# Optimization experiments

Measured on AMD Instinct MI355X. Metric: run time of the kernel, lower is better.

## Reference

```python
import jax, jax.numpy as jnp
import numpy as np

TOKENS = 1024
HIDDEN = 1024
INTER = 4096
N_EXPERTS = 8


def setup_inputs() -> dict:
    key = jax.random.key(0)
    k1, k2, k3, k4 = jax.random.split(key, 4)
    hidden_states = jax.random.normal(k1, (TOKENS, HIDDEN), dtype=jnp.float32)
    # multi-hot expert assignment mask [tokens, num_experts] with values in {0,1}
    expert_indices = jax.random.randint(k2, (TOKENS, N_EXPERTS), 0, 2, dtype=jnp.int32)
    # Phi3MLP weights per expert (Linear layers have bias=False in Phi3)
    scale_gu = 1.0 / np.sqrt(HIDDEN)
    scale_d = 1.0 / np.sqrt(INTER)
    w_gate_up = jax.random.normal(k3, (N_EXPERTS, HIDDEN, 2 * INTER), dtype=jnp.float32) * scale_gu
    w_down = jax.random.normal(k4, (N_EXPERTS, INTER, HIDDEN), dtype=jnp.float32) * scale_d
    return {
        "hidden_states": hidden_states,
        "expert_indices": expert_indices,
        "w_gate_up": w_gate_up,
        "w_down": w_down,
    }


def reference(hidden_states, expert_indices, w_gate_up, w_down):
    # Original loops per expert: gather masked tokens, run Phi3MLP, scatter-add back.
    # Mathematically equivalent dense form (jit-friendly, static shapes):
    #   out = sum_e mask[:, e] * Phi3MLP_e(x)
    # gate_up: [E, T, 2*I]
    gu = jnp.einsum('th,ehi->eti', hidden_states, w_gate_up)
    gate, up = jnp.split(gu, 2, axis=-1)  # each [E, T, I]
    act = up * jax.nn.silu(gate)          # Phi3MLP: up * silu(gate)
    y = jnp.einsum('eti,eih->eth', act, w_down)  # [E, T, H]
    mask = expert_indices.astype(hidden_states.dtype)  # [T, E]
    out = jnp.einsum('eth,te->th', y, mask)
    return out
```

## Files before the change

kernel.cpp:

```cpp
#include <hip/hip_runtime.h>
#include <hip/hip_bf16.h>
#include <stdint.h>

#define T_TOK 1024
#define HID   1024
#define INT_  4096
#define NE    8

typedef __attribute__((ext_vector_type(4))) float f32x4;
typedef __attribute__((ext_vector_type(8))) short short8;

__device__ int g_tok[NE][T_TOK];
__device__ int g_cnt[NE];

__device__ __forceinline__ uint32_t pack2bf(float a, float b) {
  unsigned short ua = __builtin_bit_cast(unsigned short, (__bf16)a);
  unsigned short ub = __builtin_bit_cast(unsigned short, (__bf16)b);
  return (uint32_t)ua | ((uint32_t)ub << 16);
}

__global__ void k0_compact(const int* __restrict__ mask)
{
  const int w    = threadIdx.x >> 6;
  const int lane = threadIdx.x & 63;
  if (w >= NE) return;
  const unsigned long long ltmask = (1ull << lane) - 1ull;
  int base = 0;
  #pragma unroll
  for (int c = 0; c < T_TOK / 64; ++c) {
    const int t = c * 64 + lane;
    const bool pred = mask[t * NE + w] != 0;
    const unsigned long long bal = __ballot(pred);
    if (pred) g_tok[w][base + __popcll(bal & ltmask)] = t;
    base += __popcll(bal);
  }
  if (lane == 0) g_cnt[w] = base;
}

__global__ __launch_bounds__(512, 1)
void k1_gateup(const float* __restrict__ x,
               const float* __restrict__ wgu,
               unsigned short* __restrict__ act)
{
  const int e   = blockIdx.z;
  const int cnt = g_cnt[e];
  const int mt  = blockIdx.y;
  const int t0  = mt * 256;
  if (t0 >= cnt) return;

  __shared__ char sA [256 * 64 * 2];
  __shared__ char sBg[128 * 64 * 2];
  __shared__ char sBu[128 * 64 * 2];

  const int nt   = blockIdx.x;
  const int tid  = threadIdx.x;
  const int lane = tid & 63;
  const int wv   = tid >> 6;
  const int wm   = (wv >> 2) * 128;
  const int wn   = (wv & 3) * 32;

  const float* wb = wgu + (size_t)e * HID * (2 * INT_);
  const int n0 = nt * 128;

  f32x4 accg[8][2], accu[8][2];
  #pragma unroll
  for (int i = 0; i < 8; ++i)
    #pragma unroll
    for (int j = 0; j < 2; ++j) {
      accg[i][j] = (f32x4){0.f, 0.f, 0.f, 0.f};
      accu[i][j] = (f32x4){0.f, 0.f, 0.f, 0.f};
    }

  const int a_m = tid >> 4;
  const int a_k = (tid & 15) * 4;
  const int b_n = (tid >> 4) * 4;
  const int b_k = (tid & 15) * 4;

  int tokr[8];
  #pragma unroll
  for (int p = 0; p < 8; ++p) tokr[p] = g_tok[e][t0 + p * 32 + a_m];

  for (int kt = 0; kt < HID; kt += 64) {
    #pragma unroll
    for (int p = 0; p < 8; ++p) {
      const int m = p * 32 + a_m;
      f32x4 v = *(const f32x4*)(x + (size_t)tokr[p] * HID + kt + a_k);
      uint2 w; w.x = pack2bf(v[0], v[1]); w.y = pack2bf(v[2], v[3]);
      *(uint2*)(sA + m * 128 + ((a_k * 2) ^ ((m & 7) << 4))) = w;
    }
    {
      const float* s_ = wb + (size_t)(kt + b_k) * (2 * INT_) + n0 + b_n;
      f32x4 g0 = *(const f32x4*)(s_);
      f32x4 g1 = *(const f32x4*)(s_ + (2 * INT_));
      f32x4 g2 = *(const f32x4*)(s_ + 2 * (2 * INT_));
      f32x4 g3 = *(const f32x4*)(s_ + 3 * (2 * INT_));
      f32x4 u0 = *(const f32x4*)(s_ + INT_);
      f32x4 u1 = *(const f32x4*)(s_ + INT_ + (2 * INT_));
      f32x4 u2 = *(const f32x4*)(s_ + INT_ + 2 * (2 * INT_));
      f32x4 u3 = *(const f32x4*)(s_ + INT_ + 3 * (2 * INT_));
      #pragma unroll
      for (int n = 0; n < 4; ++n) {
        const int row = b_n + n;
        const int off = row * 128 + ((b_k * 2) ^ ((row & 7) << 4));
        uint2 wg; wg.x = pack2bf(g0[n], g1[n]); wg.y = pack2bf(g2[n], g3[n]);
        *(uint2*)(sBg + off) = wg;
        uint2 wu; wu.x = pack2bf(u0[n], u1[n]); wu.y = pack2bf(u2[n], u3[n]);
        *(uint2*)(sBu + off) = wu;
      }
    }
    __syncthreads();
    #pragma unroll
    for (int ks = 0; ks < 2; ++ks) {
      const int kfb = ks * 64 + ((lane >> 4) << 4);
      short8 af[8], bg[2], bu[2];
      #pragma unroll
      for (int i = 0; i < 8; ++i) {
        const int r = wm + i * 16 + (lane & 15);
        af[i] = *(const short8*)(sA + r * 128 + (kfb ^ ((r & 7) << 4)));
      }
      #pragma unroll
      for (int j = 0; j < 2; ++j) {
        const int r = wn + j * 16 + (lane & 15);
        const int off = r * 128 + (kfb ^ ((r & 7) << 4));
        bg[j] = *(const short8*)(sBg + off);
        bu[j] = *(const short8*)(sBu + off);
      }
      #pragma unroll
      for (int i = 0; i < 8; ++i)
        #pragma unroll
        for (int j = 0; j < 2; ++j) {
          accg[i][j] = __builtin_amdgcn_mfma_f32_16x16x32_bf16(af[i], bg[j], accg[i][j], 0, 0, 0);
          accu[i][j] = __builtin_amdgcn_mfma_f32_16x16x32_bf16(af[i], bu[j], accu[i][j], 0, 0, 0);
        }
    }
    __syncthreads();
  }

  unsigned short* ab = act + (size_t)e * T_TOK * INT_;
  #pragma unroll
  for (int i = 0; i < 8; ++i) {
    #pragma unroll
    for (int r = 0; r < 4; ++r) {
      const int slot = t0 + wm + i * 16 + ((lane >> 4) << 2) + r;
      if (slot < cnt) {
        #pragma unroll
        for (int j = 0; j < 2; ++j) {
          const int col = n0 + wn + j * 16 + (lane & 15);
          const float g = accg[i][j][r];
          const float u = accu[i][j][r];
          const float s = u * g / (1.f + __expf(-g));
          ab[(size_t)slot * INT_ + col] = __builtin_bit_cast(unsigned short, (__bf16)s);
        }
      }
    }
  }
}

__global__ __launch_bounds__(512, 1)
void k2_down(const unsigned short* __restrict__ act,
             const float* __restrict__ wd,
             float* __restrict__ out)
{
  const int e   = blockIdx.z;
  const int cnt = g_cnt[e];
  const int mt  = blockIdx.y >> 2;
  const int ks4 = blockIdx.y & 3;
  const int t0  = mt * 256;
  if (t0 >= cnt) return;

  __shared__ char sA[256 * 64 * 2];
  __shared__ char sB[128 * 64 * 2];

  const int nt   = blockIdx.x;
  const int tid  = threadIdx.x;
  const int lane = tid & 63;
  const int wv   = tid >> 6;
  const int wm   = (wv >> 1) * 64;
  const int wn2  = (wv & 1) * 64;

  const unsigned short* ab = act + (size_t)e * T_TOK * INT_;
  const float* wb = wd + (size_t)e * INT_ * HID;
  const int n0 = nt * 128;

  f32x4 acc[4][4];
  #pragma unroll
  for (int i = 0; i < 4; ++i)
    #pragma unroll
    for (int j = 0; j < 4; ++j) acc[i][j] = (f32x4){0.f, 0.f, 0.f, 0.f};

  const int a_m = tid >> 3;
  const int a_k = (tid & 7) * 8;
  const int b_n = (tid >> 4) * 4;
  const int b_k = (tid & 15) * 4;

  const int kbeg = ks4 * (INT_ / 4);
  const int kend = kbeg + (INT_ / 4);

  for (int kt = kbeg; kt < kend; kt += 64) {
    #pragma unroll
    for (int p = 0; p < 4; ++p) {
      const int m = p * 64 + a_m;
      uint4 v = *(const uint4*)(ab + (size_t)(t0 + m) * INT_ + kt + a_k);
      *(uint4*)(sA + m * 128 + ((a_k * 2) ^ ((m & 7) << 4))) = v;
    }
    {
      const float* src = wb + (size_t)(kt + b_k) * HID + n0 + b_n;
      f32x4 r0 = *(const f32x4*)(src);
      f32x4 r1 = *(const f32x4*)(src + HID);
      f32x4 r2 = *(const f32x4*)(src + 2 * HID);
      f32x4 r3 = *(const f32x4*)(src + 3 * HID);
      #pragma unroll
      for (int n = 0; n < 4; ++n) {
        const int row = b_n + n;
        uint2 w; w.x = pack2bf(r0[n], r1[n]); w.y = pack2bf(r2[n], r3[n]);
        *(uint2*)(sB + row * 128 + ((b_k * 2) ^ ((row & 7) << 4))) = w;
      }
    }
    __syncthreads();
    #pragma unroll
    for (int ks = 0; ks < 2; ++ks) {
      const int kfb = ks * 64 + ((lane >> 4) << 4);
      short8 af[4], bf[4];
      #pragma unroll
      for (int i = 0; i < 4; ++i) {
        const int r = wm + i * 16 + (lane & 15);
        af[i] = *(const short8*)(sA + r * 128 + (kfb ^ ((r & 7) << 4)));
      }
      #pragma unroll
      for (int j = 0; j < 4; ++j) {
        const int r = wn2 + j * 16 + (lane & 15);
        bf[j] = *(const short8*)(sB + r * 128 + (kfb ^ ((r & 7) << 4)));
      }
      #pragma unroll
      for (int i = 0; i < 4; ++i)
        #pragma unroll
        for (int j = 0; j < 4; ++j)
          acc[i][j] = __builtin_amdgcn_mfma_f32_16x16x32_bf16(af[i], bf[j], acc[i][j], 0, 0, 0);
    }
    __syncthreads();
  }

  #pragma unroll
  for (int i = 0; i < 4; ++i) {
    #pragma unroll
    for (int r = 0; r < 4; ++r) {
      const int slot = t0 + wm + i * 16 + ((lane >> 4) << 2) + r;
      if (slot < cnt) {
        const int token = g_tok[e][slot];
        #pragma unroll
        for (int j = 0; j < 4; ++j) {
          const int col = n0 + wn2 + j * 16 + (lane & 15);
          atomicAdd(out + (size_t)token * HID + col, acc[i][j][r]);
        }
      }
    }
  }
}

extern "C" void kernel_launch(void* const* d_in, const int* in_sizes, int n_in,
                              void* d_out, int out_size, void* d_ws, size_t ws_size,
                              hipStream_t stream) {
  const float* x   = (const float*)d_in[0];
  const int*   idx = (const int*)d_in[1];
  const float* wgu = (const float*)d_in[2];
  const float* wd  = (const float*)d_in[3];
  float* out = (float*)d_out;
  unsigned short* act = (unsigned short*)d_ws;

  hipMemsetAsync(d_out, 0, (size_t)out_size * sizeof(float), stream);

  k0_compact<<<1, 512, 0, stream>>>(idx);

  dim3 g1(INT_ / 128, T_TOK / 256, NE);
  k1_gateup<<<g1, dim3(512), 0, stream>>>(x, wgu, act);

  dim3 g2(HID / 128, (T_TOK / 256) * 4, NE);
  k2_down<<<g2, dim3(512), 0, stream>>>(act, wd, out);
}
```

Before: 373.8 us.

## Load weights via global_load_lds as fp32, convert at fragment read, halve M tile

Weight tiles are now copied straight from global memory into LDS as fp32 using the async global_load_lds path, and converted to bf16 per column when MFMA fragments are read, not in registers before the LDS store. The activation buffer is written with an XOR-swizzled column order so the down kernel can load it directly into LDS with global_load_lds. The token tile shrinks from 256 to 128 rows, doubling the grid and so the number of times each weight tile is fetched. The fragment reads become strided scalar fp32 LDS loads with per-read bf16 packing, which may add LDS bank conflicts and ALU work.

```diff
diff --git a/kernel.cpp b/kernel.cpp
--- a/kernel.cpp
+++ b/kernel.cpp
@@ -17,6 +17,20 @@
   unsigned short ua = __builtin_bit_cast(unsigned short, (__bf16)a);
   unsigned short ub = __builtin_bit_cast(unsigned short, (__bf16)b);
   return (uint32_t)ua | ((uint32_t)ub << 16);
+}
+
+#define GL16(gsrc, ldst)                                                       \
+  __builtin_amdgcn_global_load_lds(                                            \
+      (const __attribute__((address_space(1))) void*)(gsrc),                   \
+      (__attribute__((address_space(3))) void*)(ldst), 16, 0, 0)
+
+__device__ __forceinline__ short8 bcol(const float* __restrict__ b32, int n, int ke) {
+  uint4 u;
+  u.x = pack2bf(b32[(ke + 0) * 128 + n], b32[(ke + 1) * 128 + n]);
+  u.y = pack2bf(b32[(ke + 2) * 128 + n], b32[(ke + 3) * 128 + n]);
+  u.z = pack2bf(b32[(ke + 4) * 128 + n], b32[(ke + 5) * 128 + n]);
+  u.w = pack2bf(b32[(ke + 6) * 128 + n], b32[(ke + 7) * 128 + n]);
+  return __builtin_bit_cast(short8, u);
 }
 
 __global__ void k0_compact(const int* __restrict__ mask)
@@ -45,26 +59,26 @@
   const int e   = blockIdx.z;
   const int cnt = g_cnt[e];
   const int mt  = blockIdx.y;
-  const int t0  = mt * 256;
+  const int t0  = mt * 128;
   if (t0 >= cnt) return;
 
-  __shared__ char sA [256 * 64 * 2];
-  __shared__ char sBg[128 * 64 * 2];
-  __shared__ char sBu[128 * 64 * 2];
+  __shared__ char  sA[128 * 64 * 2];
+  __shared__ float sBg[64 * 128];
+  __shared__ float sBu[64 * 128];
 
   const int nt   = blockIdx.x;
   const int tid  = threadIdx.x;
   const int lane = tid & 63;
   const int wv   = tid >> 6;
-  const int wm   = (wv >> 2) * 128;
+  const int wm   = (wv >> 2) * 64;
   const int wn   = (wv & 3) * 32;
 
   const float* wb = wgu + (size_t)e * HID * (2 * INT_);
   const int n0 = nt * 128;
 
-  f32x4 accg[8][2], accu[8][2];
-  #pragma unroll
-  for (int i = 0; i < 8; ++i)
+  f32x4 accg[4][2], accu[4][2];
+  #pragma unroll
+  for (int i = 0; i < 4; ++i)
     #pragma unroll
     for (int j = 0; j < 2; ++j) {
       accg[i][j] = (f32x4){0.f, 0.f, 0.f, 0.f};
@@ -73,60 +87,48 @@
 
   const int a_m = tid >> 4;
   const int a_k = (tid & 15) * 4;
-  const int b_n = (tid >> 4) * 4;
-  const int b_k = (tid & 15) * 4;
-
-  int tokr[8];
-  #pragma unroll
-  for (int p = 0; p < 8; ++p) tokr[p] = g_tok[e][t0 + p * 32 + a_m];
+  int tokr[4];
+  #pragma unroll
+  for (int p = 0; p < 4; ++p) tokr[p] = g_tok[e][t0 + p * 32 + a_m];
+
+  const int bkw = wv * 2;
+  const int bkl = (lane >> 5);
+  const int bnc = (lane & 31) * 4;
 
   for (int kt = 0; kt < HID; kt += 64) {
     #pragma unroll
-    for (int p = 0; p < 8; ++p) {
+    for (int s = 0; s < 4; ++s) {
+      const int krow = s * 16 + bkw;
+      const float* sg = wb + (size_t)(kt + krow + bkl) * (2 * INT_) + n0 + bnc;
+      GL16(sg,         (char*)sBg + krow * 512);
+      GL16(sg + INT_,  (char*)sBu + krow * 512);
+    }
+    #pragma unroll
+    for (int p = 0; p < 4; ++p) {
       const int m = p * 32 + a_m;
       f32x4 v = *(const f32x4*)(x + (size_t)tokr[p] * HID + kt + a_k);
       uint2 w; w.x = pack2bf(v[0], v[1]); w.y = pack2bf(v[2], v[3]);
       *(uint2*)(sA + m * 128 + ((a_k * 2) ^ ((m & 7) << 4))) = w;
     }
-    {
-      const float* s_ = wb + (size_t)(kt + b_k) * (2 * INT_) + n0 + b_n;
-      f32x4 g0 = *(const f32x4*)(s_);
-      f32x4 g1 = *(const f32x4*)(s_ + (2 * INT_));
-      f32x4 g2 = *(const f32x4*)(s_ + 2 * (2 * INT_));
-      f32x4 g3 = *(const f32x4*)(s_ + 3 * (2 * INT_));
-      f32x4 u0 = *(const f32x4*)(s_ + INT_);
-      f32x4 u1 = *(const f32x4*)(s_ + INT_ + (2 * INT_));
-      f32x4 u2 = *(const f32x4*)(s_ + INT_ + 2 * (2 * INT_));
-      f32x4 u3 = *(const f32x4*)(s_ + INT_ + 3 * (2 * INT_));
-      #pragma unroll
-      for (int n = 0; n < 4; ++n) {
-        const int row = b_n + n;
-        const int off = row * 128 + ((b_k * 2) ^ ((row & 7) << 4));
-        uint2 wg; wg.x = pack2bf(g0[n], g1[n]); wg.y = pack2bf(g2[n], g3[n]);
-        *(uint2*)(sBg + off) = wg;
-        uint2 wu; wu.x = pack2bf(u0[n], u1[n]); wu.y = pack2bf(u2[n], u3[n]);
-        *(uint2*)(sBu + off) = wu;
-      }
-    }
     __syncthreads();
     #pragma unroll
     for (int ks = 0; ks < 2; ++ks) {
       const int kfb = ks * 64 + ((lane >> 4) << 4);
-      short8 af[8], bg[2], bu[2];
-      #pragma unroll
-      for (int i = 0; i < 8; ++i) {
+      const int ke  = ks * 32 + ((lane >> 4) << 3);
+      short8 af[4], bg[2], bu[2];
+      #pragma unroll
+      for (int i = 0; i < 4; ++i) {
         const int r = wm + i * 16 + (lane & 15);
         af[i] = *(const short8*)(sA + r * 128 + (kfb ^ ((r & 7) << 4)));
       }
       #pragma unroll
       for (int j = 0; j < 2; ++j) {
-        const int r = wn + j * 16 + (lane & 15);
-        const int off = r * 128 + (kfb ^ ((r & 7) << 4));
-        bg[j] = *(const short8*)(sBg + off);
-        bu[j] = *(const short8*)(sBu + off);
-      }
-      #pragma unroll
-      for (int i = 0; i < 8; ++i)
+        const int n = wn + j * 16 + (lane & 15);
+        bg[j] = bcol(sBg, n, ke);
+        bu[j] = bcol(sBu, n, ke);
+      }
+      #pragma unroll
+      for (int i = 0; i < 4; ++i)
         #pragma unroll
         for (int j = 0; j < 2; ++j) {
           accg[i][j] = __builtin_amdgcn_mfma_f32_16x16x32_bf16(af[i], bg[j], accg[i][j], 0, 0, 0);
@@ -138,7 +140,7 @@
 
   unsigned short* ab = act + (size_t)e * T_TOK * INT_;
   #pragma unroll
-  for (int i = 0; i < 8; ++i) {
+  for (int i = 0; i < 4; ++i) {
     #pragma unroll
     for (int r = 0; r < 4; ++r) {
       const int slot = t0 + wm + i * 16 + ((lane >> 4) << 2) + r;
@@ -146,10 +148,12 @@
         #pragma unroll
         for (int j = 0; j < 2; ++j) {
           const int col = n0 + wn + j * 16 + (lane & 15);
+          const int cw  = (col >> 3) & 7;
+          const int colS = (col & ~56) | (((cw ^ (slot & 7)) & 7) << 3);
           const float g = accg[i][j][r];
           const float u = accu[i][j][r];
           const float s = u * g / (1.f + __expf(-g));
-          ab[(size_t)slot * INT_ + col] = __builtin_bit_cast(unsigned short, (__bf16)s);
+          ab[(size_t)slot * INT_ + colS] = __builtin_bit_cast(unsigned short, (__bf16)s);
         }
       }
     }
@@ -165,76 +169,70 @@
   const int cnt = g_cnt[e];
   const int mt  = blockIdx.y >> 2;
   const int ks4 = blockIdx.y & 3;
-  const int t0  = mt * 256;
+  const int t0  = mt * 128;
   if (t0 >= cnt) return;
 
-  __shared__ char sA[256 * 64 * 2];
-  __shared__ char sB[128 * 64 * 2];
+  __shared__ char  sA[128 * 64 * 2];
+  __shared__ float sB[64 * 128];
 
   const int nt   = blockIdx.x;
   const int tid  = threadIdx.x;
   const int lane = tid & 63;
   const int wv   = tid >> 6;
-  const int wm   = (wv >> 1) * 64;
-  const int wn2  = (wv & 1) * 64;
+  const int wm   = (wv >> 2) * 64;
+  const int wn   = (wv & 3) * 32;
 
   const unsigned short* ab = act + (size_t)e * T_TOK * INT_;
   const float* wb = wd + (size_t)e * INT_ * HID;
   const int n0 = nt * 128;
 
-  f32x4 acc[4][4];
+  f32x4 acc[4][2];
   #pragma unroll
   for (int i = 0; i < 4; ++i)
     #pragma unroll
-    for (int j = 0; j < 4; ++j) acc[i][j] = (f32x4){0.f, 0.f, 0.f, 0.f};
-
-  const int a_m = tid >> 3;
-  const int a_k = (tid & 7) * 8;
-  const int b_n = (tid >> 4) * 4;
-  const int b_k = (tid & 15) * 4;
+    for (int j = 0; j < 2; ++j) acc[i][j] = (f32x4){0.f, 0.f, 0.f, 0.f};
+
+  const int bkw = wv * 2;
+  const int bkl = (lane >> 5);
+  const int bnc = (lane & 31) * 4;
 
   const int kbeg = ks4 * (INT_ / 4);
   const int kend = kbeg + (INT_ / 4);
 
   for (int kt = kbeg; kt < kend; kt += 64) {
     #pragma unroll
-    for (int p = 0; p < 4; ++p) {
-      const int m = p * 64 + a_m;
-      uint4 v = *(const uint4*)(ab + (size_t)(t0 + m) * INT_ + kt + a_k);
-      *(uint4*)(sA + m * 128 + ((a_k * 2) ^ ((m & 7) << 4))) = v;
-    }
-    {
-      const float* src = wb + (size_t)(kt + b_k) * HID + n0 + b_n;
-      f32x4 r0 = *(const f32x4*)(src);
-      f32x4 r1 = *(const f32x4*)(src + HID);
-      f32x4 r2 = *(const f32x4*)(src + 2 * HID);
-      f32x4 r3 = *(const f32x4*)(src + 3 * HID);
-      #pragma unroll
-      for (int n = 0; n < 4; ++n) {
-        const int row = b_n + n;
-        uint2 w; w.x = pack2bf(r0[n], r1[n]); w.y = pack2bf(r2[n], r3[n]);
-        *(uint2*)(sB + row * 128 + ((b_k * 2) ^ ((row & 7) << 4))) = w;
-      }
+    for (int s = 0; s < 2; ++s) {
+      const int mrow = s * 64 + wv * 8;
+      const unsigned short* srcA =
+          ab + (size_t)(t0 + mrow + (lane >> 3)) * INT_ + kt + (lane & 7) * 8;
+      GL16(srcA, (char*)sA + mrow * 128);
+    }
+    #pragma unroll
+    for (int s = 0; s < 4; ++s) {
+      const int krow = s * 16 + bkw;
+      const float* srcB = wb + (size_t)(kt + krow + bkl) * HID + n0 + bnc;
+      GL16(srcB, (char*)sB + krow * 512);
     }
     __syncthreads();
     #pragma unroll
     for (int ks = 0; ks < 2; ++ks) {
       const int kfb = ks * 64 + ((lane >> 4) << 4);
-      short8 af[4], bf[4];
+      const int ke  = ks * 32 + ((lane >> 4) << 3);
+      short8 af[4], bf[2];
       #pragma unroll
       for (int i = 0; i < 4; ++i) {
         const int r = wm + i * 16 + (lane & 15);
         af[i] = *(const short8*)(sA + r * 128 + (kfb ^ ((r & 7) << 4)));
       }
       #pragma unroll
-      for (int j = 0; j < 4; ++j) {
-        const int r = wn2 + j * 16 + (lane & 15);
-        bf[j] = *(const short8*)(sB + r * 128 + (kfb ^ ((r & 7) << 4)));
+      for (int j = 0; j < 2; ++j) {
+        const int n = wn + j * 16 + (lane & 15);
+        bf[j] = bcol(sB, n, ke);
       }
       #pragma unroll
       for (int i = 0; i < 4; ++i)
         #pragma unroll
-        for (int j = 0; j < 4; ++j)
+        for (int j = 0; j < 2; ++j)
           acc[i][j] = __builtin_amdgcn_mfma_f32_16x16x32_bf16(af[i], bf[j], acc[i][j], 0, 0, 0);
     }
     __syncthreads();
@@ -248,8 +246,8 @@
       if (slot < cnt) {
         const int token = g_tok[e][slot];
         #pragma unroll
-        for (int j = 0; j < 4; ++j) {
-          const int col = n0 + wn2 + j * 16 + (lane & 15);
+        for (int j = 0; j < 2; ++j) {
+          const int col = n0 + wn + j * 16 + (lane & 15);
           atomicAdd(out + (size_t)token * HID + col, acc[i][j][r]);
         }
       }
@@ -271,9 +269,9 @@
 
   k0_compact<<<1, 512, 0, stream>>>(idx);
 
-  dim3 g1(INT_ / 128, T_TOK / 256, NE);
+  dim3 g1(INT_ / 128, T_TOK / 128, NE);
   k1_gateup<<<g1, dim3(512), 0, stream>>>(x, wgu, act);
 
-  dim3 g2(HID / 128, (T_TOK / 256) * 4, NE);
+  dim3 g2(HID / 128, (T_TOK / 128) * 4, NE);
   k2_down<<<g2, dim3(512), 0, stream>>>(act, wd, out);
 }
```

New measurement: 414.7 us. 11.0% more time.

## Pre-convert inputs to transposed bf16 and stream tiles into LDS directly

Applied to the files above, without the earlier changes.

Adds kernels that convert x to bf16 and transpose-convert both expert weight tensors to bf16, K-contiguous layouts in workspace on every call. The GEMM kernels then fill LDS with `global_load_lds` 16-byte transfers, XOR-swizzled to match the existing fragment reads, replacing per-thread fp32 loads plus in-register packing. The down-projection kernel also moves to 128-token tiles with 256 threads and two blocks per CU. The aim is to cut conversion and register-staging work inside the GEMM loops and make tile loads coalesced, at the cost of an extra full read and write of the weights in the conversion passes.

```diff
diff --git a/kernel.cpp b/kernel.cpp
--- a/kernel.cpp
+++ b/kernel.cpp
@@ -18,6 +18,11 @@
   unsigned short ub = __builtin_bit_cast(unsigned short, (__bf16)b);
   return (uint32_t)ua | ((uint32_t)ub << 16);
 }
+
+#define GL16(gsrc, ldst)                                                       \
+  __builtin_amdgcn_global_load_lds(                                            \
+      (const __attribute__((address_space(1))) void*)(gsrc),                   \
+      (__attribute__((address_space(3))) void*)(ldst), 16, 0, 0)
 
 __global__ void k0_compact(const int* __restrict__ mask)
 {
@@ -37,9 +42,55 @@
   if (lane == 0) g_cnt[w] = base;
 }
 
+__global__ void cvt_x(const float* __restrict__ xin, unsigned short* __restrict__ xout)
+{
+  const int i = (blockIdx.x * 256 + threadIdx.x) * 8;
+  f32x4 a = *(const f32x4*)(xin + i);
+  f32x4 b = *(const f32x4*)(xin + i + 4);
+  uint4 u;
+  u.x = pack2bf(a[0], a[1]); u.y = pack2bf(a[2], a[3]);
+  u.z = pack2bf(b[0], b[1]); u.w = pack2bf(b[2], b[3]);
+  *(uint4*)(xout + i) = u;
+}
+
+__global__ void cvt_T(const float* __restrict__ in, unsigned short* __restrict__ out,
+                      int R, int C)
+{
+  __shared__ float tile[64][65];
+  const int e  = blockIdx.z;
+  const int c0 = blockIdx.x * 64;
+  const int r0 = blockIdx.y * 64;
+  const float*    ip = in  + (size_t)e * R * C;
+  unsigned short* op = out + (size_t)e * R * C;
+  const int t  = threadIdx.x;
+  const int rr = t >> 4, c4 = (t & 15) * 4;
+  #pragma unroll
+  for (int s = 0; s < 4; ++s) {
+    f32x4 v = *(const f32x4*)(ip + (size_t)(r0 + s * 16 + rr) * C + c0 + c4);
+    tile[s * 16 + rr][c4 + 0] = v[0];
+    tile[s * 16 + rr][c4 + 1] = v[1];
+    tile[s * 16 + rr][c4 + 2] = v[2];
+    tile[s * 16 + rr][c4 + 3] = v[3];
+  }
+  __syncthreads();
+  const int c = t >> 2, rs = (t & 3) * 16;
+  uint4 u0, u1;
+  u0.x = pack2bf(tile[rs + 0][c],  tile[rs + 1][c]);
+  u0.y = pack2bf(tile[rs + 2][c],  tile[rs + 3][c]);
+  u0.z = pack2bf(tile[rs + 4][c],  tile[rs + 5][c]);
+  u0.w = pack2bf(tile[rs + 6][c],  tile[rs + 7][c]);
+  u1.x = pack2bf(tile[rs + 8][c],  tile[rs + 9][c]);
+  u1.y = pack2bf(tile[rs + 10][c], tile[rs + 11][c]);
+  u1.z = pack2bf(tile[rs + 12][c], tile[rs + 13][c]);
+  u1.w = pack2bf(tile[rs + 14][c], tile[rs + 15][c]);
+  unsigned short* orow = op + (size_t)(c0 + c) * R + r0 + rs;
+  *(uint4*)(orow)     = u0;
+  *(uint4*)(orow + 8) = u1;
+}
+
 __global__ __launch_bounds__(512, 1)
-void k1_gateup(const float* __restrict__ x,
-               const float* __restrict__ wgu,
+void k1_gateup(const unsigned short* __restrict__ xb,
+               const unsigned short* __restrict__ wguT,
                unsigned short* __restrict__ act)
 {
   const int e   = blockIdx.z;
@@ -48,9 +99,9 @@
   const int t0  = mt * 256;
   if (t0 >= cnt) return;
 
-  __shared__ char sA [256 * 64 * 2];
-  __shared__ char sBg[128 * 64 * 2];
-  __shared__ char sBu[128 * 64 * 2];
+  __shared__ char sA [256 * 128];
+  __shared__ char sBg[128 * 128];
+  __shared__ char sBu[128 * 128];
 
   const int nt   = blockIdx.x;
   const int tid  = threadIdx.x;
@@ -58,9 +109,10 @@
   const int wv   = tid >> 6;
   const int wm   = (wv >> 2) * 128;
   const int wn   = (wv & 3) * 32;
-
-  const float* wb = wgu + (size_t)e * HID * (2 * INT_);
-  const int n0 = nt * 128;
+  const int n0   = nt * 128;
+
+  const unsigned short* wg = wguT + (size_t)e * 8192 * HID + (size_t)n0 * HID;
+  const unsigned short* wu = wg + (size_t)4096 * HID;
 
   f32x4 accg[8][2], accu[8][2];
   #pragma unroll
@@ -71,42 +123,25 @@
       accu[i][j] = (f32x4){0.f, 0.f, 0.f, 0.f};
     }
 
-  const int a_m = tid >> 4;
-  const int a_k = (tid & 15) * 4;
-  const int b_n = (tid >> 4) * 4;
-  const int b_k = (tid & 15) * 4;
-
-  int tokr[8];
-  #pragma unroll
-  for (int p = 0; p < 8; ++p) tokr[p] = g_tok[e][t0 + p * 32 + a_m];
+  const int drow  = lane >> 3;
+  const int dchk8 = (((lane & 7) ^ drow) << 3);
+
+  int tokA[4];
+  #pragma unroll
+  for (int s = 0; s < 4; ++s)
+    tokA[s] = g_tok[e][t0 + (s * 8 + wv) * 8 + drow];
 
   for (int kt = 0; kt < HID; kt += 64) {
     #pragma unroll
-    for (int p = 0; p < 8; ++p) {
-      const int m = p * 32 + a_m;
-      f32x4 v = *(const f32x4*)(x + (size_t)tokr[p] * HID + kt + a_k);
-      uint2 w; w.x = pack2bf(v[0], v[1]); w.y = pack2bf(v[2], v[3]);
-      *(uint2*)(sA + m * 128 + ((a_k * 2) ^ ((m & 7) << 4))) = w;
-    }
-    {
-      const float* s_ = wb + (size_t)(kt + b_k) * (2 * INT_) + n0 + b_n;
-      f32x4 g0 = *(const f32x4*)(s_);
-      f32x4 g1 = *(const f32x4*)(s_ + (2 * INT_));
-      f32x4 g2 = *(const f32x4*)(s_ + 2 * (2 * INT_));
-      f32x4 g3 = *(const f32x4*)(s_ + 3 * (2 * INT_));
-      f32x4 u0 = *(const f32x4*)(s_ + INT_);
-      f32x4 u1 = *(const f32x4*)(s_ + INT_ + (2 * INT_));
-      f32x4 u2 = *(const f32x4*)(s_ + INT_ + 2 * (2 * INT_));
-      f32x4 u3 = *(const f32x4*)(s_ + INT_ + 3 * (2 * INT_));
-      #pragma unroll
-      for (int n = 0; n < 4; ++n) {
-        const int row = b_n + n;
-        const int off = row * 128 + ((b_k * 2) ^ ((row & 7) << 4));
-        uint2 wg; wg.x = pack2bf(g0[n], g1[n]); wg.y = pack2bf(g2[n], g3[n]);
-        *(uint2*)(sBg + off) = wg;
-        uint2 wu; wu.x = pack2bf(u0[n], u1[n]); wu.y = pack2bf(u2[n], u3[n]);
-        *(uint2*)(sBu + off) = wu;
-      }
+    for (int s = 0; s < 4; ++s) {
+      const int rb = (s * 8 + wv) * 8;
+      GL16(xb + (size_t)tokA[s] * HID + kt + dchk8, sA + rb * 128);
+    }
+    #pragma unroll
+    for (int s = 0; s < 2; ++s) {
+      const int rb = (s * 8 + wv) * 8;
+      GL16(wg + (size_t)(rb + drow) * HID + kt + dchk8, sBg + rb * 128);
+      GL16(wu + (size_t)(rb + drow) * HID + kt + dchk8, sBu + rb * 128);
     }
     __syncthreads();
     #pragma unroll
@@ -156,31 +191,31 @@
   }
 }
 
-__global__ __launch_bounds__(512, 1)
+__global__ __launch_bounds__(256, 2)
 void k2_down(const unsigned short* __restrict__ act,
-             const float* __restrict__ wd,
+             const unsigned short* __restrict__ wdT,
              float* __restrict__ out)
 {
   const int e   = blockIdx.z;
   const int cnt = g_cnt[e];
   const int mt  = blockIdx.y >> 2;
   const int ks4 = blockIdx.y & 3;
-  const int t0  = mt * 256;
+  const int t0  = mt * 128;
   if (t0 >= cnt) return;
 
-  __shared__ char sA[256 * 64 * 2];
-  __shared__ char sB[128 * 64 * 2];
+  __shared__ char sA[128 * 128];
+  __shared__ char sB[128 * 128];
 
   const int nt   = blockIdx.x;
   const int tid  = threadIdx.x;
   const int lane = tid & 63;
   const int wv   = tid >> 6;
   const int wm   = (wv >> 1) * 64;
-  const int wn2  = (wv & 1) * 64;
+  const int wn   = (wv & 1) * 64;
+  const int n0   = nt * 128;
 
   const unsigned short* ab = act + (size_t)e * T_TOK * INT_;
-  const float* wb = wd + (size_t)e * INT_ * HID;
-  const int n0 = nt * 128;
+  const unsigned short* wb = wdT + (size_t)e * HID * INT_ + (size_t)n0 * INT_;
 
   f32x4 acc[4][4];
   #pragma unroll
@@ -188,33 +223,17 @@
     #pragma unroll
     for (int j = 0; j < 4; ++j) acc[i][j] = (f32x4){0.f, 0.f, 0.f, 0.f};
 
-  const int a_m = tid >> 3;
-  const int a_k = (tid & 7) * 8;
-  const int b_n = (tid >> 4) * 4;
-  const int b_k = (tid & 15) * 4;
+  const int drow  = lane >> 3;
+  const int dchk8 = (((lane & 7) ^ drow) << 3);
 
   const int kbeg = ks4 * (INT_ / 4);
-  const int kend = kbeg + (INT_ / 4);
-
-  for (int kt = kbeg; kt < kend; kt += 64) {
-    #pragma unroll
-    for (int p = 0; p < 4; ++p) {
-      const int m = p * 64 + a_m;
-      uint4 v = *(const uint4*)(ab + (size_t)(t0 + m) * INT_ + kt + a_k);
-      *(uint4*)(sA + m * 128 + ((a_k * 2) ^ ((m & 7) << 4))) = v;
-    }
-    {
-      const float* src = wb + (size_t)(kt + b_k) * HID + n0 + b_n;
-      f32x4 r0 = *(const f32x4*)(src);
-      f32x4 r1 = *(const f32x4*)(src + HID);
-      f32x4 r2 = *(const f32x4*)(src + 2 * HID);
-      f32x4 r3 = *(const f32x4*)(src + 3 * HID);
-      #pragma unroll
-      for (int n = 0; n < 4; ++n) {
-        const int row = b_n + n;
-        uint2 w; w.x = pack2bf(r0[n], r1[n]); w.y = pack2bf(r2[n], r3[n]);
-        *(uint2*)(sB + row * 128 + ((b_k * 2) ^ ((row & 7) << 4))) = w;
-      }
+
+  for (int kt = kbeg; kt < kbeg + INT_ / 4; kt += 64) {
+    #pragma unroll
+    for (int s = 0; s < 4; ++s) {
+      const int rb = (s * 4 + wv) * 8;
+      GL16(ab + (size_t)(t0 + rb + drow) * INT_ + kt + dchk8, sA + rb * 128);
+      GL16(wb + (size_t)(rb + drow) * INT_ + kt + dchk8, sB + rb * 128);
     }
     __syncthreads();
     #pragma unroll
@@ -228,7 +247,7 @@
       }
       #pragma unroll
       for (int j = 0; j < 4; ++j) {
-        const int r = wn2 + j * 16 + (lane & 15);
+        const int r = wn + j * 16 + (lane & 15);
         bf[j] = *(const short8*)(sB + r * 128 + (kfb ^ ((r & 7) << 4)));
       }
       #pragma unroll
@@ -249,7 +268,7 @@
         const int token = g_tok[e][slot];
         #pragma unroll
         for (int j = 0; j < 4; ++j) {
-          const int col = n0 + wn2 + j * 16 + (lane & 15);
+          const int col = n0 + wn + j * 16 + (lane & 15);
           atomicAdd(out + (size_t)token * HID + col, acc[i][j][r]);
         }
       }
@@ -265,15 +284,23 @@
   const float* wgu = (const float*)d_in[2];
   const float* wd  = (const float*)d_in[3];
   float* out = (float*)d_out;
-  unsigned short* act = (unsigned short*)d_ws;
+
+  char* ws = (char*)d_ws;
+  unsigned short* act  = (unsigned short*)(ws);
+  unsigned short* xb16 = (unsigned short*)(ws + 67108864);
+  unsigned short* wguT = (unsigned short*)(ws + 69206016);
+  unsigned short* wdT  = (unsigned short*)(ws + 203423744);
 
   hipMemsetAsync(d_out, 0, (size_t)out_size * sizeof(float), stream);
 
   k0_compact<<<1, 512, 0, stream>>>(idx);
+  cvt_x<<<T_TOK * HID / (256 * 8), 256, 0, stream>>>(x, xb16);
+  cvt_T<<<dim3(8192 / 64, 1024 / 64, NE), 256, 0, stream>>>(wgu, wguT, 1024, 8192);
+  cvt_T<<<dim3(1024 / 64, 4096 / 64, NE), 256, 0, stream>>>(wd, wdT, 4096, 1024);
 
   dim3 g1(INT_ / 128, T_TOK / 256, NE);
-  k1_gateup<<<g1, dim3(512), 0, stream>>>(x, wgu, act);
-
-  dim3 g2(HID / 128, (T_TOK / 256) * 4, NE);
-  k2_down<<<g2, dim3(512), 0, stream>>>(act, wd, out);
-}
+  k1_gateup<<<g1, dim3(512), 0, stream>>>(xb16, wguT, act);
+
+  dim3 g2(HID / 128, (T_TOK / 128) * 4, NE);
+  k2_down<<<g2, dim3(256), 0, stream>>>(act, wdT, out);
+}
```

Result: faster. 366.4 us (-2.0%).
